# Kernel tuning notes

Hardware: AMD Instinct MI355X
Metric: run time of the kernel (lower is better)

Reference implementation:

```python
import jax, jax.numpy as jnp
import numpy as np

VX, VY, VZ = 128, 128, 128  # BEV voxel grid (z collapsed by the pooling kernel)
B = 2
N_CAMS = 6


def setup_inputs() -> dict:
    key = jax.random.key(0)
    k1, k2, k3 = jax.random.split(key, 3)
    depth_logits = jax.random.normal(k1, (B * N_CAMS, 112, 16, 44), dtype=jnp.float32)
    context = jax.random.normal(k2, (B * N_CAMS, 80, 16, 44), dtype=jnp.float32)
    geom_xyz = jax.random.randint(k3, (B, N_CAMS, 112, 16, 44, 3), 0, 128, dtype=jnp.int32)
    return {"depth_logits": depth_logits, "context": context, "geom_xyz": geom_xyz}


def reference(depth_logits, context, geom_xyz):
    # depth_logits: (B*N, D, H, W); context: (B*N, C, H, W); geom_xyz: (B, N, D, H, W, 3) int
    BN, D, H, W = depth_logits.shape
    C = context.shape[1]
    b = geom_xyz.shape[0]
    n = BN // b

    # depth distribution (softmax over depth bins), as in DepthNet output
    depth = jax.nn.softmax(depth_logits, axis=1)  # (BN, D, H, W)

    # lift: outer product depth x context -> (BN, C, D, H, W)
    feat = depth[:, None, :, :, :] * context[:, :, None, :, :]

    # arrange as (B, P, C) with P = N*D*H*W frustum points
    feat = feat.reshape(b, n, C, D, H, W).transpose(0, 1, 3, 4, 5, 2).reshape(b, -1, C)
    g = geom_xyz.reshape(b, -1, 3)  # (B, P, 3) int voxel coords

    # range check (kernel skips out-of-grid points); z only range-checked, not indexed
    bounds = jnp.array([VX, VY, VZ], dtype=g.dtype)
    valid = jnp.all((g >= 0) & (g < bounds), axis=-1)  # (B, P)
    dump = VX * VY  # overflow bucket for invalid points
    idx = jnp.where(valid, g[..., 1] * VX + g[..., 0], dump)  # (B, P)

    def pool(f, i):  # f: (P, C), i: (P,)
        return jax.ops.segment_sum(f, i, num_segments=VX * VY + 1)[: VX * VY]

    bev = jax.vmap(pool)(feat, idx)  # (B, VX*VY, C)
    return bev.reshape(b, VY, VX, C).transpose(0, 3, 1, 2)  # (B, C, VY, VX)
```

## Files before the change

### kernel.cpp

```cpp
#include <hip/hip_runtime.h>
#include <hip/hip_bf16.h>
#include <math.h>

#define BATCH 2
#define NCAM 6
#define BN_TOT (BATCH * NCAM)
#define DBINS 112
#define HH 16
#define WW 44
#define CCH 80
#define VXD 128
#define VYD 128
#define HWD (HH * WW)
#define NCELL (VXD * VYD)
#define NCELL_TOT (BATCH * NCELL)
#define NCOLS (BN_TOT * HWD)
#define NPTS (NCOLS * DBINS)
#define DCHUNK 28

#define NBLK_PREP 264
#define PREP_PTS 3584
#define NBUCKET 1024
#define FLATN (NBUCKET * NBLK_PREP)
#define SOLVE_CAP 1280

#define WS_CTXT_OFF    0u
#define WS_CTXT_BYTES  ((unsigned)NCOLS * CCH * 4u)
#define WS_PC_OFF      (WS_CTXT_OFF + WS_CTXT_BYTES)
#define WS_PC_BYTES    ((unsigned)NPTS * 8u)
#define WS_PLIST_OFF   (WS_PC_OFF + WS_PC_BYTES)
#define WS_PLIST_BYTES ((unsigned)NPTS * 8u)
#define WS_CNT_OFF     (WS_PLIST_OFF + WS_PLIST_BYTES)
#define WS_CNT_BYTES   ((unsigned)FLATN * 4u)
#define WS_TOT_OFF     (WS_CNT_OFF + WS_CNT_BYTES)
#define WS_TOT_BYTES   ((unsigned)NBUCKET * 4u)
#define WS_BST_OFF     (WS_TOT_OFF + WS_TOT_BYTES)
#define WS_BST_BYTES   4128u
#define WS_NEED        (WS_BST_OFF + WS_BST_BYTES)

__global__ __launch_bounds__(128) void prep_kernel(
    const float* __restrict__ depth_logits,
    const int*   __restrict__ geom,
    int2* __restrict__ pc,
    int*  __restrict__ counts) {
  __shared__ float sred[4][32];
  __shared__ int shist[NBUCKET];
  const int t = threadIdx.x;
  for (int i = t; i < NBUCKET; i += 128) shist[i] = 0;

  const int col_l = t & 31;
  const int chunk = t >> 5;
  const int blk = blockIdx.x;
  const int bn = blk / 22;
  const int tile22 = blk - bn * 22;
  const int hw = tile22 * 32 + col_l;
  const int b = bn / NCAM;
  const int col = bn * HWD + hw;

  const float* lp =
      depth_logits + ((size_t)bn * DBINS + chunk * DCHUNK) * HWD + hw;
  float v[DCHUNK];
  float m = -INFINITY;
#pragma unroll
  for (int j = 0; j < DCHUNK; ++j) {
    v[j] = lp[(size_t)j * HWD];
    m = fmaxf(m, v[j]);
  }
  sred[chunk][col_l] = m;
  __syncthreads();
  m = fmaxf(fmaxf(sred[0][col_l], sred[1][col_l]),
            fmaxf(sred[2][col_l], sred[3][col_l]));
  float lsum = 0.0f;
#pragma unroll
  for (int j = 0; j < DCHUNK; ++j) {
    v[j] = __expf(v[j] - m);
    lsum += v[j];
  }
  __syncthreads();
  sred[chunk][col_l] = lsum;
  __syncthreads();
  const float inv = 1.0f / (sred[0][col_l] + sred[1][col_l] +
                            sred[2][col_l] + sred[3][col_l]);

  const int* gp = geom + (((size_t)bn * DBINS + chunk * DCHUNK) * HWD + hw) * 3;
#pragma unroll 4
  for (int j = 0; j < DCHUNK; ++j) {
    const int x = gp[(size_t)j * HWD * 3 + 0];
    const int y = gp[(size_t)j * HWD * 3 + 1];
    const int z = gp[(size_t)j * HWD * 3 + 2];
    int cell = -1;
    if (((unsigned)x < (unsigned)VXD) & ((unsigned)y < (unsigned)VYD) &
        ((unsigned)z < 128u)) {
      cell = (b << 14) + (y << 7) + x;
      atomicAdd(&shist[cell >> 5], 1);
    }
    pc[(size_t)(chunk * DCHUNK + j) * NCOLS + col] =
        make_int2(cell, __float_as_int(v[j] * inv));
  }
  __syncthreads();
  for (int i = t; i < NBUCKET; i += 128) counts[i * NBLK_PREP + blk] = shist[i];
}

__global__ __launch_bounds__(256) void ctxt_kernel(
    const float* __restrict__ context, float* __restrict__ ctxT) {
  __shared__ float tile[CCH][65];
  const int blk = blockIdx.x;
  const int bn = blk / 11;
  const int hw0 = (blk - bn * 11) * 64;
  const float* src = context + (size_t)bn * CCH * HWD + hw0;
  for (int p = threadIdx.x; p < CCH * 64; p += 256) {
    const int c = p >> 6;
    const int i = p & 63;
    tile[c][i] = src[(size_t)c * HWD + i];
  }
  __syncthreads();
  float* dst = ctxT + (size_t)(bn * HWD + hw0) * CCH;
  for (int p = threadIdx.x; p < CCH * 64; p += 256) {
    const int i = p / CCH;
    const int c = p - i * CCH;
    dst[p] = tile[c][i];
  }
}

__global__ __launch_bounds__(320) void scanA_kernel(
    int* __restrict__ counts, int* __restrict__ totals) {
  __shared__ int s[NBLK_PREP];
  const int t = threadIdx.x;
  const int k = blockIdx.x;
  int orig = 0;
  if (t < NBLK_PREP) {
    orig = counts[k * NBLK_PREP + t];
    s[t] = orig;
  }
  __syncthreads();
  for (int d = 1; d < NBLK_PREP; d <<= 1) {
    int v = 0;
    if (t < NBLK_PREP && t >= d) v = s[t - d];
    __syncthreads();
    if (t < NBLK_PREP) s[t] += v;
    __syncthreads();
  }
  if (t < NBLK_PREP) counts[k * NBLK_PREP + t] = s[t] - orig;
  if (t == NBLK_PREP - 1) totals[k] = s[t];
}

__global__ __launch_bounds__(1024) void scanB_kernel(
    const int* __restrict__ totals, int* __restrict__ bucketStart) {
  __shared__ int wpart[16];
  const int t = threadIdx.x;
  const int lane = t & 63;
  const int wid = t >> 6;
  const int v = totals[t];
  int incl = v;
#pragma unroll
  for (int d = 1; d < 64; d <<= 1) {
    const int u = __shfl_up(incl, d, 64);
    if (lane >= d) incl += u;
  }
  if (lane == 63) wpart[wid] = incl;
  __syncthreads();
  if (t < 16) {
    const int w = wpart[t];
    int iw = w;
#pragma unroll
    for (int d = 1; d < 16; d <<= 1) {
      const int u = __shfl_up(iw, d, 16);
      if (t >= d) iw += u;
    }
    wpart[t] = iw - w;
  }
  __syncthreads();
  const int ex = wpart[wid] + incl - v;
  bucketStart[t] = ex;
  if (t == 1023) bucketStart[NBUCKET] = ex + v;
}

__global__ __launch_bounds__(256) void partition_kernel(
    const int2* __restrict__ pc,
    const int*  __restrict__ offsets,
    const int*  __restrict__ bucketStart,
    int2* __restrict__ plist) {
  __shared__ int hist[NBUCKET], hoff[NBUCKET], hcur[NBUCKET], gdst[NBUCKET];
  __shared__ int2 stag[PREP_PTS];
  __shared__ int gaddr[PREP_PTS];
  __shared__ int wpart2[4];
  const int t = threadIdx.x;
  const int blk = blockIdx.x;
  const int bn = blk / 22;
  const int tile22 = blk - bn * 22;
  const int colbase = bn * HWD + tile22 * 32;

  for (int i = t; i < NBUCKET; i += 256) hist[i] = 0;
  __syncthreads();

  int2 pay[14];
  int  bkt[14];
#pragma unroll
  for (int j = 0; j < 14; ++j) {
    const int p = t + j * 256;
    const int d = p >> 5;
    const int col = colbase + (p & 31);
    const int2 pp = pc[(size_t)d * NCOLS + col];
    int bk = -1;
    if (pp.x >= 0) {
      bk = pp.x >> 5;
      atomicAdd(&hist[bk], 1);
      pay[j] = make_int2(((pp.x & 31) << 14) | col, pp.y);
    }
    bkt[j] = bk;
  }
  __syncthreads();

  const int lane = t & 63, wid = t >> 6;
  const int h0 = hist[4 * t], h1 = hist[4 * t + 1];
  const int h2 = hist[4 * t + 2], h3 = hist[4 * t + 3];
  const int s4 = h0 + h1 + h2 + h3;
  int incl = s4;
#pragma unroll
  for (int d = 1; d < 64; d <<= 1) {
    const int u = __shfl_up(incl, d, 64);
    if (lane >= d) incl += u;
  }
  if (lane == 63) wpart2[wid] = incl;
  __syncthreads();
  int wbase = 0;
  if (wid == 1) wbase = wpart2[0];
  else if (wid == 2) wbase = wpart2[0] + wpart2[1];
  else if (wid == 3) wbase = wpart2[0] + wpart2[1] + wpart2[2];
  const int ex = wbase + incl - s4;
  hoff[4 * t] = ex;
  hoff[4 * t + 1] = ex + h0;
  hoff[4 * t + 2] = ex + h0 + h1;
  hoff[4 * t + 3] = ex + h0 + h1 + h2;
  hcur[4 * t] = 0; hcur[4 * t + 1] = 0; hcur[4 * t + 2] = 0; hcur[4 * t + 3] = 0;
#pragma unroll
  for (int i = 0; i < 4; ++i) {
    const int bb = 4 * t + i;
    gdst[bb] = bucketStart[bb] + offsets[bb * NBLK_PREP + blk];
  }
  __syncthreads();

#pragma unroll
  for (int j = 0; j < 14; ++j) {
    if (bkt[j] >= 0) {
      const int r = atomicAdd(&hcur[bkt[j]], 1);
      const int pos = hoff[bkt[j]] + r;
      stag[pos] = pay[j];
      gaddr[pos] = gdst[bkt[j]] + r;
    }
  }
  __syncthreads();

  const int nval = hoff[NBUCKET - 1] + hist[NBUCKET - 1];
  for (int i = t; i < nval; i += 256) {
    plist[gaddr[i]] = stag[i];
  }
}

__global__ __launch_bounds__(256) void solve_kernel(
    const int*  __restrict__ bucketStart,
    const int2* __restrict__ plist,
    const float* __restrict__ ctxT,
    float* __restrict__ out) {
  __shared__ int2 spts[SOLVE_CAP];
  __shared__ float tile[32 * 81];
  __shared__ int hist[32], starts[33], cur[32];
  const int t = threadIdx.x;
  const int k = blockIdx.x;
  const int b = k >> 9;
  const int y = (k & 511) >> 2;
  const int x0 = (k & 3) << 5;
  const int bs = bucketStart[k];
  const int be = bucketStart[k + 1];
  const int n_all = be - bs;
  const int n = min(n_all, SOLVE_CAP);

  if (t < 32) hist[t] = 0;
  __syncthreads();

  int2 rp[5];
  int nper = 0;
#pragma unroll
  for (int j = 0; j < 5; ++j) {
    const int i = t + j * 256;
    if (i < n) {
      const int2 p = plist[bs + i];
      rp[j] = p;
      atomicAdd(&hist[(p.x >> 14) & 31], 1);
      nper = j + 1;
    }
  }
  __syncthreads();

  const int lane = t & 63, wid = t >> 6;
  if (t < 32) {
    const int h = hist[t];
    int incl = h;
#pragma unroll
    for (int d = 1; d < 32; d <<= 1) {
      const int u = __shfl_up(incl, d, 32);
      if (t >= d) incl += u;
    }
    starts[t] = incl - h;
    cur[t] = incl - h;
    if (t == 31) starts[32] = incl;
  }
  __syncthreads();

#pragma unroll
  for (int j = 0; j < 5; ++j) {
    if (j < nper) {
      const int key = (rp[j].x >> 14) & 31;
      const int r = atomicAdd(&cur[key], 1);
      spts[r] = rp[j];
    }
  }
  __syncthreads();

  for (int ci = 0; ci < 8; ++ci) {
    const int xl = wid * 8 + ci;
    const int s0 = starts[xl];
    const int s1 = starts[xl + 1];
    float a0 = 0.0f, a1 = 0.0f;
    int i = s0;
    for (; i + 4 <= s1; i += 4) {
      const int2 p0 = spts[i], p1 = spts[i + 1], p2 = spts[i + 2], p3 = spts[i + 3];
      const float* c0 = ctxT + (size_t)(p0.x & 0x3FFF) * CCH;
      const float* c1 = ctxT + (size_t)(p1.x & 0x3FFF) * CCH;
      const float* c2 = ctxT + (size_t)(p2.x & 0x3FFF) * CCH;
      const float* c3 = ctxT + (size_t)(p3.x & 0x3FFF) * CCH;
      const float q0 = __int_as_float(p0.y), q1 = __int_as_float(p1.y);
      const float q2 = __int_as_float(p2.y), q3 = __int_as_float(p3.y);
      const float f0 = c0[lane], f1 = c1[lane], f2 = c2[lane], f3 = c3[lane];
      a0 = fmaf(q0, f0, a0);
      a0 = fmaf(q1, f1, a0);
      a0 = fmaf(q2, f2, a0);
      a0 = fmaf(q3, f3, a0);
      if (lane < CCH - 64) {
        a1 = fmaf(q0, c0[64 + lane], a1);
        a1 = fmaf(q1, c1[64 + lane], a1);
        a1 = fmaf(q2, c2[64 + lane], a1);
        a1 = fmaf(q3, c3[64 + lane], a1);
      }
    }
    for (; i < s1; ++i) {
      const int2 p = spts[i];
      const float pr = __int_as_float(p.y);
      const float* cb = ctxT + (size_t)(p.x & 0x3FFF) * CCH;
      a0 = fmaf(pr, cb[lane], a0);
      if (lane < CCH - 64) a1 = fmaf(pr, cb[64 + lane], a1);
    }
    tile[xl * 81 + lane] = a0;
    if (lane < CCH - 64) tile[xl * 81 + 64 + lane] = a1;
  }

  for (int i = SOLVE_CAP; i < n_all; ++i) {
    const int2 p = plist[bs + i];
    const int key = (p.x >> 14) & 31;
    if ((key >> 3) == wid) {
      const float pr = __int_as_float(p.y);
      const float* cb = ctxT + (size_t)(p.x & 0x3FFF) * CCH;
      tile[key * 81 + lane] += pr * cb[lane];
      if (lane < CCH - 64) tile[key * 81 + 64 + lane] += pr * cb[64 + lane];
    }
  }
  __syncthreads();

  float* dst = out + (((size_t)(b * CCH)) << 14) + (y << 7) + x0;
  for (int p = t; p < CCH * 32; p += 256) {
    const int c = p >> 5;
    const int xl = p & 31;
    dst[((size_t)c << 14) + xl] = tile[xl * 81 + c];
  }
}

__global__ __launch_bounds__(256) void lift_scatter_kernel(
    const float* __restrict__ depth_logits, const float* __restrict__ context,
    const int* __restrict__ geom, float* __restrict__ accum) {
  __shared__ float sred[256];
  __shared__ float sprob[DBINS];
  __shared__ float sctx[CCH];
  __shared__ int   scell[DBINS];

  const int blk = blockIdx.x;
  const int bn  = blk / HWD;
  const int hw  = blk - bn * HWD;
  const int b   = bn / NCAM;
  const int t   = threadIdx.x;

  float v = -INFINITY;
  if (t < DBINS) v = depth_logits[(size_t)bn * DBINS * HWD + (size_t)t * HWD + hw];
  sred[t] = v;
  __syncthreads();
  for (int s = 128; s > 0; s >>= 1) {
    if (t < s) sred[t] = fmaxf(sred[t], sred[t + s]);
    __syncthreads();
  }
  const float m = sred[0];
  __syncthreads();
  float e = 0.0f;
  if (t < DBINS) e = __expf(v - m);
  sred[t] = e;
  __syncthreads();
  for (int s = 128; s > 0; s >>= 1) {
    if (t < s) sred[t] += sred[t + s];
    __syncthreads();
  }
  if (t < DBINS) sprob[t] = e / sred[0];
  if (t < CCH) sctx[t] = context[((size_t)bn * CCH + t) * HWD + hw];
  if (t < DBINS) {
    const size_t gbase = (((size_t)bn * DBINS + t) * HWD + hw) * 3;
    const int x = geom[gbase + 0];
    const int y = geom[gbase + 1];
    const int z = geom[gbase + 2];
    scell[t] = (x >= 0 && x < VXD && y >= 0 && y < VYD && z >= 0 && z < 128)
                   ? y * VXD + x : -1;
  }
  __syncthreads();

  float* __restrict__ base = accum + (((size_t)b * CCH) << 14);
  int d = t / CCH;
  int c = t - d * CCH;
#pragma unroll
  for (int k = 0; k < 35; ++k) {
    const int cell = scell[d];
    if (cell >= 0) {
      unsafeAtomicAdd(base + (((size_t)c) << 14) + cell, sprob[d] * sctx[c]);
    }
    d += 3; c += 16;
    if (c >= CCH) { c -= CCH; d += 1; }
  }
}

extern "C" void kernel_launch(void* const* d_in, const int* in_sizes, int n_in,
                              void* d_out, int out_size, void* d_ws, size_t ws_size,
                              hipStream_t stream) {
  const float* depth_logits = (const float*)d_in[0];
  const float* context      = (const float*)d_in[1];
  const int*   geom         = (const int*)d_in[2];
  float* out = (float*)d_out;
  char* ws = (char*)d_ws;

  if (ws_size >= WS_NEED) {
    float* ctxT   = (float*)(ws + WS_CTXT_OFF);
    int2*  pc     = (int2*)(ws + WS_PC_OFF);
    int2*  plist  = (int2*)(ws + WS_PLIST_OFF);
    int*   counts = (int*)(ws + WS_CNT_OFF);
    int*   totals = (int*)(ws + WS_TOT_OFF);
    int*   bstart = (int*)(ws + WS_BST_OFF);

    prep_kernel<<<NBLK_PREP, 128, 0, stream>>>(depth_logits, geom, pc, counts);
    ctxt_kernel<<<BN_TOT * 11, 256, 0, stream>>>(context, ctxT);
    scanA_kernel<<<NBUCKET, 320, 0, stream>>>(counts, totals);
    scanB_kernel<<<1, 1024, 0, stream>>>(totals, bstart);
    partition_kernel<<<NBLK_PREP, 256, 0, stream>>>(pc, counts, bstart, plist);
    solve_kernel<<<NBUCKET, 256, 0, stream>>>(bstart, plist, ctxT, out);
  } else {
    hipMemsetAsync(d_out, 0, (size_t)out_size * sizeof(float), stream);
    lift_scatter_kernel<<<BN_TOT * HWD, 256, 0, stream>>>(
        depth_logits, context, geom, out);
  }
}
```

Before: 131.2 us.

## Fuse context transpose into prep, fold bucket scan into partition, split solve blocks

The context transpose now happens inside prep_kernel, and the separate scanB kernel is gone. Every partition block redoes the 1024-entry prefix scan over bucket totals, and block 0 writes bucketStart. solve_kernel launches twice as many blocks, each handling 16 x-columns instead of 32. The aim is fewer launches and more parallelism in the solve stage. The cost is redundant scan work, duplicate plist reads in each half-block, and extra shared memory in prep.

```diff
diff --git a/kernel.cpp b/kernel.cpp
--- a/kernel.cpp
+++ b/kernel.cpp
@@ -40,11 +40,14 @@
 
 __global__ __launch_bounds__(128) void prep_kernel(
     const float* __restrict__ depth_logits,
+    const float* __restrict__ context,
     const int*   __restrict__ geom,
-    int2* __restrict__ pc,
-    int*  __restrict__ counts) {
+    int2*  __restrict__ pc,
+    float* __restrict__ ctxT,
+    int*   __restrict__ counts) {
   __shared__ float sred[4][32];
   __shared__ int shist[NBUCKET];
+  __shared__ float ctile[32][CCH + 1];
   const int t = threadIdx.x;
   for (int i = t; i < NBUCKET; i += 128) shist[i] = 0;
 
@@ -53,9 +56,17 @@
   const int blk = blockIdx.x;
   const int bn = blk / 22;
   const int tile22 = blk - bn * 22;
-  const int hw = tile22 * 32 + col_l;
+  const int hw0 = tile22 * 32;
+  const int hw = hw0 + col_l;
   const int b = bn / NCAM;
   const int col = bn * HWD + hw;
+
+  const float* csrc = context + (size_t)bn * CCH * HWD + hw0;
+  for (int p = t; p < 32 * CCH; p += 128) {
+    const int c = p >> 5;
+    const int i2 = p & 31;
+    ctile[i2][c] = csrc[(size_t)c * HWD + i2];
+  }
 
   const float* lp =
       depth_logits + ((size_t)bn * DBINS + chunk * DCHUNK) * HWD + hw;
@@ -99,26 +110,12 @@
   }
   __syncthreads();
   for (int i = t; i < NBUCKET; i += 128) counts[i * NBLK_PREP + blk] = shist[i];
-}
-
-__global__ __launch_bounds__(256) void ctxt_kernel(
-    const float* __restrict__ context, float* __restrict__ ctxT) {
-  __shared__ float tile[CCH][65];
-  const int blk = blockIdx.x;
-  const int bn = blk / 11;
-  const int hw0 = (blk - bn * 11) * 64;
-  const float* src = context + (size_t)bn * CCH * HWD + hw0;
-  for (int p = threadIdx.x; p < CCH * 64; p += 256) {
-    const int c = p >> 6;
-    const int i = p & 63;
-    tile[c][i] = src[(size_t)c * HWD + i];
-  }
-  __syncthreads();
-  float* dst = ctxT + (size_t)(bn * HWD + hw0) * CCH;
-  for (int p = threadIdx.x; p < CCH * 64; p += 256) {
-    const int i = p / CCH;
-    const int c = p - i * CCH;
-    dst[p] = tile[c][i];
+
+  float* cdst = ctxT + (size_t)(bn * HWD + hw0) * CCH;
+  for (int p = t; p < 32 * CCH; p += 128) {
+    const int i2 = p / CCH;
+    const int c = p - i2 * CCH;
+    cdst[p] = ctile[i2][c];
   }
 }
 
@@ -144,46 +141,16 @@
   if (t == NBLK_PREP - 1) totals[k] = s[t];
 }
 
-__global__ __launch_bounds__(1024) void scanB_kernel(
-    const int* __restrict__ totals, int* __restrict__ bucketStart) {
-  __shared__ int wpart[16];
-  const int t = threadIdx.x;
-  const int lane = t & 63;
-  const int wid = t >> 6;
-  const int v = totals[t];
-  int incl = v;
-#pragma unroll
-  for (int d = 1; d < 64; d <<= 1) {
-    const int u = __shfl_up(incl, d, 64);
-    if (lane >= d) incl += u;
-  }
-  if (lane == 63) wpart[wid] = incl;
-  __syncthreads();
-  if (t < 16) {
-    const int w = wpart[t];
-    int iw = w;
-#pragma unroll
-    for (int d = 1; d < 16; d <<= 1) {
-      const int u = __shfl_up(iw, d, 16);
-      if (t >= d) iw += u;
-    }
-    wpart[t] = iw - w;
-  }
-  __syncthreads();
-  const int ex = wpart[wid] + incl - v;
-  bucketStart[t] = ex;
-  if (t == 1023) bucketStart[NBUCKET] = ex + v;
-}
-
 __global__ __launch_bounds__(256) void partition_kernel(
     const int2* __restrict__ pc,
     const int*  __restrict__ offsets,
-    const int*  __restrict__ bucketStart,
+    const int*  __restrict__ totals,
+    int*  __restrict__ bucketStart,
     int2* __restrict__ plist) {
   __shared__ int hist[NBUCKET], hoff[NBUCKET], hcur[NBUCKET], gdst[NBUCKET];
   __shared__ int2 stag[PREP_PTS];
   __shared__ int gaddr[PREP_PTS];
-  __shared__ int wpart2[4];
+  __shared__ int wpartA[4], wpartB[4];
   const int t = threadIdx.x;
   const int blk = blockIdx.x;
   const int bn = blk / 22;
@@ -212,31 +179,60 @@
   __syncthreads();
 
   const int lane = t & 63, wid = t >> 6;
+
   const int h0 = hist[4 * t], h1 = hist[4 * t + 1];
   const int h2 = hist[4 * t + 2], h3 = hist[4 * t + 3];
   const int s4 = h0 + h1 + h2 + h3;
-  int incl = s4;
+  int inclA = s4;
 #pragma unroll
   for (int d = 1; d < 64; d <<= 1) {
-    const int u = __shfl_up(incl, d, 64);
-    if (lane >= d) incl += u;
-  }
-  if (lane == 63) wpart2[wid] = incl;
-  __syncthreads();
-  int wbase = 0;
-  if (wid == 1) wbase = wpart2[0];
-  else if (wid == 2) wbase = wpart2[0] + wpart2[1];
-  else if (wid == 3) wbase = wpart2[0] + wpart2[1] + wpart2[2];
-  const int ex = wbase + incl - s4;
-  hoff[4 * t] = ex;
-  hoff[4 * t + 1] = ex + h0;
-  hoff[4 * t + 2] = ex + h0 + h1;
-  hoff[4 * t + 3] = ex + h0 + h1 + h2;
+    const int u = __shfl_up(inclA, d, 64);
+    if (lane >= d) inclA += u;
+  }
+  if (lane == 63) wpartA[wid] = inclA;
+
+  const int u0 = totals[4 * t], u1 = totals[4 * t + 1];
+  const int u2 = totals[4 * t + 2], u3 = totals[4 * t + 3];
+  const int su = u0 + u1 + u2 + u3;
+  __syncthreads();
+
+  int wbaseA = 0;
+  if (wid == 1) wbaseA = wpartA[0];
+  else if (wid == 2) wbaseA = wpartA[0] + wpartA[1];
+  else if (wid == 3) wbaseA = wpartA[0] + wpartA[1] + wpartA[2];
+  const int exA = wbaseA + inclA - s4;
+  hoff[4 * t] = exA;
+  hoff[4 * t + 1] = exA + h0;
+  hoff[4 * t + 2] = exA + h0 + h1;
+  hoff[4 * t + 3] = exA + h0 + h1 + h2;
   hcur[4 * t] = 0; hcur[4 * t + 1] = 0; hcur[4 * t + 2] = 0; hcur[4 * t + 3] = 0;
-#pragma unroll
-  for (int i = 0; i < 4; ++i) {
-    const int bb = 4 * t + i;
-    gdst[bb] = bucketStart[bb] + offsets[bb * NBLK_PREP + blk];
+
+  int inclB = su;
+#pragma unroll
+  for (int d = 1; d < 64; d <<= 1) {
+    const int u = __shfl_up(inclB, d, 64);
+    if (lane >= d) inclB += u;
+  }
+  if (lane == 63) wpartB[wid] = inclB;
+  __syncthreads();
+
+  int wbaseB = 0;
+  if (wid == 1) wbaseB = wpartB[0];
+  else if (wid == 2) wbaseB = wpartB[0] + wpartB[1];
+  else if (wid == 3) wbaseB = wpartB[0] + wpartB[1] + wpartB[2];
+  const int exB = wbaseB + inclB - su;
+  const int bv0 = exB, bv1 = exB + u0, bv2 = exB + u0 + u1,
+            bv3 = exB + u0 + u1 + u2;
+  gdst[4 * t]     = bv0 + offsets[(4 * t)     * NBLK_PREP + blk];
+  gdst[4 * t + 1] = bv1 + offsets[(4 * t + 1) * NBLK_PREP + blk];
+  gdst[4 * t + 2] = bv2 + offsets[(4 * t + 2) * NBLK_PREP + blk];
+  gdst[4 * t + 3] = bv3 + offsets[(4 * t + 3) * NBLK_PREP + blk];
+  if (blk == 0) {
+    bucketStart[4 * t] = bv0;
+    bucketStart[4 * t + 1] = bv1;
+    bucketStart[4 * t + 2] = bv2;
+    bucketStart[4 * t + 3] = bv3;
+    if (t == 255) bucketStart[NBUCKET] = bv3 + u3;
   }
   __syncthreads();
 
@@ -263,62 +259,66 @@
     const float* __restrict__ ctxT,
     float* __restrict__ out) {
   __shared__ int2 spts[SOLVE_CAP];
-  __shared__ float tile[32 * 81];
-  __shared__ int hist[32], starts[33], cur[32];
+  __shared__ float tile[16 * 81];
+  __shared__ int hist[16], starts[17], cur[16];
   const int t = threadIdx.x;
-  const int k = blockIdx.x;
-  const int b = k >> 9;
-  const int y = (k & 511) >> 2;
-  const int x0 = (k & 3) << 5;
-  const int bs = bucketStart[k];
-  const int be = bucketStart[k + 1];
+  const int kb = blockIdx.x >> 1;
+  const int half = blockIdx.x & 1;
+  const int b = kb >> 9;
+  const int y = (kb & 511) >> 2;
+  const int x0 = ((kb & 3) << 5) + (half << 4);
+  const int bs = bucketStart[kb];
+  const int be = bucketStart[kb + 1];
   const int n_all = be - bs;
   const int n = min(n_all, SOLVE_CAP);
 
-  if (t < 32) hist[t] = 0;
+  if (t < 16) hist[t] = 0;
   __syncthreads();
 
   int2 rp[5];
-  int nper = 0;
+  int  rk[5];
 #pragma unroll
   for (int j = 0; j < 5; ++j) {
+    rk[j] = -1;
     const int i = t + j * 256;
     if (i < n) {
       const int2 p = plist[bs + i];
-      rp[j] = p;
-      atomicAdd(&hist[(p.x >> 14) & 31], 1);
-      nper = j + 1;
+      const int key = (p.x >> 14) & 31;
+      if ((key >> 4) == half) {
+        rp[j] = p;
+        rk[j] = key & 15;
+        atomicAdd(&hist[key & 15], 1);
+      }
     }
   }
   __syncthreads();
 
   const int lane = t & 63, wid = t >> 6;
-  if (t < 32) {
+  if (t < 16) {
     const int h = hist[t];
     int incl = h;
 #pragma unroll
-    for (int d = 1; d < 32; d <<= 1) {
-      const int u = __shfl_up(incl, d, 32);
+    for (int d = 1; d < 16; d <<= 1) {
+      const int u = __shfl_up(incl, d, 16);
       if (t >= d) incl += u;
     }
     starts[t] = incl - h;
     cur[t] = incl - h;
-    if (t == 31) starts[32] = incl;
+    if (t == 15) starts[16] = incl;
   }
   __syncthreads();
 
 #pragma unroll
   for (int j = 0; j < 5; ++j) {
-    if (j < nper) {
-      const int key = (rp[j].x >> 14) & 31;
-      const int r = atomicAdd(&cur[key], 1);
+    if (rk[j] >= 0) {
+      const int r = atomicAdd(&cur[rk[j]], 1);
       spts[r] = rp[j];
     }
   }
   __syncthreads();
 
-  for (int ci = 0; ci < 8; ++ci) {
-    const int xl = wid * 8 + ci;
+  for (int ci = 0; ci < 4; ++ci) {
+    const int xl = wid * 4 + ci;
     const int s0 = starts[xl];
     const int s1 = starts[xl + 1];
     float a0 = 0.0f, a1 = 0.0f;
@@ -357,19 +357,19 @@
   for (int i = SOLVE_CAP; i < n_all; ++i) {
     const int2 p = plist[bs + i];
     const int key = (p.x >> 14) & 31;
-    if ((key >> 3) == wid) {
+    if ((key >> 4) == half && (((key & 15) >> 2) == wid)) {
       const float pr = __int_as_float(p.y);
       const float* cb = ctxT + (size_t)(p.x & 0x3FFF) * CCH;
-      tile[key * 81 + lane] += pr * cb[lane];
-      if (lane < CCH - 64) tile[key * 81 + 64 + lane] += pr * cb[64 + lane];
+      tile[(key & 15) * 81 + lane] += pr * cb[lane];
+      if (lane < CCH - 64) tile[(key & 15) * 81 + 64 + lane] += pr * cb[64 + lane];
     }
   }
   __syncthreads();
 
   float* dst = out + (((size_t)(b * CCH)) << 14) + (y << 7) + x0;
-  for (int p = t; p < CCH * 32; p += 256) {
-    const int c = p >> 5;
-    const int xl = p & 31;
+  for (int p = t; p < CCH * 16; p += 256) {
+    const int c = p >> 4;
+    const int xl = p & 15;
     dst[((size_t)c << 14) + xl] = tile[xl * 81 + c];
   }
 }
@@ -449,12 +449,12 @@
     int*   totals = (int*)(ws + WS_TOT_OFF);
     int*   bstart = (int*)(ws + WS_BST_OFF);
 
-    prep_kernel<<<NBLK_PREP, 128, 0, stream>>>(depth_logits, geom, pc, counts);
-    ctxt_kernel<<<BN_TOT * 11, 256, 0, stream>>>(context, ctxT);
+    prep_kernel<<<NBLK_PREP, 128, 0, stream>>>(depth_logits, context, geom,
+                                               pc, ctxT, counts);
     scanA_kernel<<<NBUCKET, 320, 0, stream>>>(counts, totals);
-    scanB_kernel<<<1, 1024, 0, stream>>>(totals, bstart);
-    partition_kernel<<<NBLK_PREP, 256, 0, stream>>>(pc, counts, bstart, plist);
-    solve_kernel<<<NBUCKET, 256, 0, stream>>>(bstart, plist, ctxT, out);
+    partition_kernel<<<NBLK_PREP, 256, 0, stream>>>(pc, counts, totals,
+                                                    bstart, plist);
+    solve_kernel<<<NBUCKET * 2, 256, 0, stream>>>(bstart, plist, ctxT, out);
   } else {
     hipMemsetAsync(d_out, 0, (size_t)out_size * sizeof(float), stream);
     lift_scatter_kernel<<<BN_TOT * HWD, 256, 0, stream>>>(
```

Result: faster. 123.4 us (-5.9%).
